# Performance work log

Measured on AMD Instinct MI355X. Metric: run time of the kernel, lower is better.

The kernel has to match this reference:

```python
import jax, jax.numpy as jnp
import numpy as np

H = 16  # num_heads
EPS = 1e-5

def _ln(x, g, b):
    m = jnp.mean(x, axis=-1, keepdims=True)
    v = jnp.var(x, axis=-1, keepdims=True)
    return (x - m) * jax.lax.rsqrt(v + EPS) * g + b

def setup_inputs() -> dict:
    key = jax.random.key(0)
    ks = jax.random.split(key, 4)
    B, N, C = 4, 1024, 1024
    D = C // H
    s_in = (2.0 / (C + 3 * C)) ** 0.5  # xavier-ish
    s_pr = (2.0 / (C + C)) ** 0.5
    return {
        "x": jax.random.normal(ks[0], (B, N, C), dtype=jnp.float32),
        "W_qkv": jax.random.normal(ks[1], (3 * C, C), dtype=jnp.float32) * s_in,
        "b_qkv": jnp.zeros((3 * C,), dtype=jnp.float32),
        "qn_g": jnp.ones((D,), dtype=jnp.float32),
        "qn_b": jnp.zeros((D,), dtype=jnp.float32),
        "kn_g": jnp.ones((D,), dtype=jnp.float32),
        "kn_b": jnp.zeros((D,), dtype=jnp.float32),
        "W_proj": jax.random.normal(ks[2], (C, C), dtype=jnp.float32) * s_pr,
        "b_proj": jnp.zeros((C,), dtype=jnp.float32),
    }

def reference(x, W_qkv, b_qkv, qn_g, qn_b, kn_g, kn_b, W_proj, b_proj):
    B, N, C = x.shape
    D = C // H
    scale = D ** -0.5
    qkv = x @ W_qkv.T + b_qkv                       # [B,N,3C]
    qkv = qkv.reshape(B, N, 3, H, D).transpose(2, 0, 3, 1, 4)  # [3,B,H,N,D]
    q, k, v = qkv[0], qkv[1], qkv[2]
    # source bug: qk_norm=(False,) is truthy -> LayerNorm applied to q and k
    q = _ln(q, qn_g, qn_b) * scale
    k = _ln(k, kn_g, kn_b)
    attn = jnp.einsum('bhnd,bhmd->bhnm', q, k)       # [B,H,N,N]
    weights = jax.nn.softmax(attn, axis=-1)
    out = jnp.einsum('bhnm,bhmd->bhnd', weights, v)  # [B,H,N,D]
    out = out.transpose(0, 2, 1, 3).reshape(B, N, C)
    out = out @ W_proj.T + b_proj
    return (out, weights)
```

## Files before the change

kernel.cpp:

```cpp
#include <hip/hip_runtime.h>
#include <math.h>

#define NH 16
#define HD 64
#define NB 4
#define SQ 1024
#define CH 1024

typedef _Float16 f16x8  __attribute__((ext_vector_type(8)));
typedef _Float16 f16x4  __attribute__((ext_vector_type(4)));
typedef float    f32x4  __attribute__((ext_vector_type(4)));

typedef const __attribute__((address_space(1))) void gvoid_t;
typedef __attribute__((address_space(3))) void lvoid_t;

#define NQ_X   (NB * SQ * CH / 4)
#define NQ_WQ  (3 * CH * CH / 4)
#define NQ_WP  (CH * CH / 4)
__global__ __launch_bounds__(256) void k_split_all(
    const float* __restrict__ x, const float* __restrict__ wqkv,
    const float* __restrict__ wp,
    _Float16* __restrict__ xf, _Float16* __restrict__ wqf,
    _Float16* __restrict__ wpf)
{
    int i = blockIdx.x * 256 + threadIdx.x;
    const float4 v = (i < NQ_X) ? ((const float4*)x)[i]
                   : (i < NQ_X + NQ_WQ) ? ((const float4*)wqkv)[i - NQ_X]
                   : ((const float4*)wp)[i - NQ_X - NQ_WQ];
    f16x4 h;
    h[0] = (_Float16)v.x; h[1] = (_Float16)v.y;
    h[2] = (_Float16)v.z; h[3] = (_Float16)v.w;
    if (i < NQ_X)             ((f16x4*)xf)[i] = h;
    else if (i < NQ_X + NQ_WQ)((f16x4*)wqf)[i - NQ_X] = h;
    else                      ((f16x4*)wpf)[i - NQ_X - NQ_WQ] = h;
}

template<int EPI>
__global__ __launch_bounds__(256) void k_mfma_gemm(
    const _Float16* __restrict__ A, const _Float16* __restrict__ B,
    const float* __restrict__ bias, float* __restrict__ outp,
    _Float16* __restrict__ qf, _Float16* __restrict__ kf, _Float16* __restrict__ vTf,
    const float* __restrict__ qg, const float* __restrict__ qb_,
    const float* __restrict__ kg, const float* __restrict__ kb_)
{
    __shared__ __align__(16) _Float16 sA[128 * 32];
    __shared__ __align__(16) _Float16 sB[128 * 32];

    const int tid = threadIdx.x;
    const int wid = tid >> 6, lane = tid & 63;
    const int wr = wid >> 1, wc = wid & 1;
    const int m0 = blockIdx.y * 128, n0 = blockIdx.x * 128;

    f32x4 acc[4][4];
    #pragma unroll
    for (int i = 0; i < 4; ++i)
        #pragma unroll
        for (int j = 0; j < 4; ++j)
            acc[i][j] = (f32x4){0.f, 0.f, 0.f, 0.f};

    const _Float16* gsrc = (wid < 2) ? A : B;
    _Float16* sdst = (wid < 2) ? sA : sB;
    const int gbase = (wid < 2) ? m0 : n0;
    const int ibase = (wid & 1) * 4;
    const int grow = gbase + (lane >> 2);
    const int gcol = (lane & 3) * 8;

    const int arow = wr * 64 + (lane & 15);
    const int brow = wc * 64 + (lane & 15);
    const int koff = (lane >> 4) * 8;

    for (int k0 = 0; k0 < CH; k0 += 32) {
        #pragma unroll
        for (int i = 0; i < 4; ++i) {
            const _Float16* g = gsrc + (size_t)(grow + (ibase + i) * 16) * CH + k0 + gcol;
            __builtin_amdgcn_global_load_lds((gvoid_t*)g,
                                             (lvoid_t*)(sdst + (ibase + i) * 512),
                                             16, 0, 0);
        }
        __syncthreads();

        f16x8 a[4], b[4];
        #pragma unroll
        for (int f = 0; f < 4; ++f) {
            a[f] = *(const f16x8*)&sA[(arow + f * 16) * 32 + koff];
            b[f] = *(const f16x8*)&sB[(brow + f * 16) * 32 + koff];
        }
        #pragma unroll
        for (int i = 0; i < 4; ++i)
            #pragma unroll
            for (int j = 0; j < 4; ++j)
                acc[i][j] = __builtin_amdgcn_mfma_f32_16x16x32_f16(a[i], b[j], acc[i][j], 0, 0, 0);
        __syncthreads();
    }

    const int crow = (lane >> 4) * 4;
    const int ccol = lane & 15;

    if (EPI == 1) {
        #pragma unroll
        for (int i = 0; i < 4; ++i) {
            #pragma unroll
            for (int j = 0; j < 4; ++j) {
                const int n = n0 + wc * 64 + j * 16 + ccol;
                const float bv = bias[n];
                #pragma unroll
                for (int r = 0; r < 4; ++r) {
                    const int m = m0 + wr * 64 + i * 16 + crow + r;
                    outp[(size_t)m * CH + n] = acc[i][j][r] + bv;
                }
            }
        }
    } else {
        const int nblk = n0 + wc * 64;
        const int sec = nblk >> 10;
        const int h = (nblk & 1023) >> 6;
        float bv[4];
        #pragma unroll
        for (int j = 0; j < 4; ++j) bv[j] = bias[nblk + j * 16 + ccol];

        if (sec < 2) {
            const float* gp = (sec == 0) ? qg : kg;
            const float* bp = (sec == 0) ? qb_ : kb_;
            float g4[4], b4[4];
            #pragma unroll
            for (int j = 0; j < 4; ++j) { g4[j] = gp[j*16+ccol]; b4[j] = bp[j*16+ccol]; }
            const float scale = (sec == 0) ? 0.125f : 1.0f;
            _Float16* dst = (sec == 0) ? qf : kf;
            #pragma unroll
            for (int i = 0; i < 4; ++i) {
                #pragma unroll
                for (int r = 0; r < 4; ++r) {
                    const int m = m0 + wr * 64 + i * 16 + crow + r;
                    const int b_ = m >> 10, nn = m & 1023;
                    float vals[4], s = 0.f, q2 = 0.f;
                    #pragma unroll
                    for (int j = 0; j < 4; ++j) {
                        vals[j] = acc[i][j][r] + bv[j];
                        s += vals[j]; q2 += vals[j] * vals[j];
                    }
                    #pragma unroll
                    for (int o = 1; o < 16; o <<= 1) {
                        s  += __shfl_xor(s, o, 64);
                        q2 += __shfl_xor(q2, o, 64);
                    }
                    const float mean = s * 0.015625f;
                    const float var = q2 * 0.015625f - mean * mean;
                    const float rstd = rsqrtf(var + 1e-5f);
                    #pragma unroll
                    for (int j = 0; j < 4; ++j) {
                        const float y = ((vals[j] - mean) * rstd * g4[j] + b4[j]) * scale;
                        dst[((size_t)(b_ * NH + h) * SQ + nn) * HD + j * 16 + ccol] = (_Float16)y;
                    }
                }
            }
        } else {
            #pragma unroll
            for (int i = 0; i < 4; ++i) {
                const int m0r = m0 + wr * 64 + i * 16 + crow;
                const int b_ = m0r >> 10, nn0 = m0r & 1023;
                #pragma unroll
                for (int j = 0; j < 4; ++j) {
                    f16x4 tmp;
                    #pragma unroll
                    for (int r = 0; r < 4; ++r) tmp[r] = (_Float16)(acc[i][j][r] + bv[j]);
                    *(f16x4*)&vTf[((size_t)(b_ * NH + h) * HD + j * 16 + ccol) * SQ + nn0] = tmp;
                }
            }
        }
    }
}

__global__ __launch_bounds__(256) void k_attn(
    const _Float16* __restrict__ q, const _Float16* __restrict__ k,
    const _Float16* __restrict__ vT, float* __restrict__ W,
    _Float16* __restrict__ opf)
{
    __shared__ _Float16 Pl[4][32][40];
    __shared__ float Of[4][32][72];
    const int L = blockIdx.x;
    const int bh   = (L & 7) * 8 + (L >> 6);
    const int xblk = (L >> 3) & 7;
    const int wid = threadIdx.x >> 6, lane = threadIdx.x & 63;
    const int row0 = xblk * 128 + wid * 32;
    const int lr = lane & 15, lg = lane >> 4;

    const _Float16* qh = q  + (size_t)bh * SQ * HD;
    const _Float16* kh = k  + (size_t)bh * SQ * HD;
    const _Float16* vh = vT + (size_t)bh * HD * SQ;

    f16x8 qb[2][2];
    #pragma unroll
    for (int qf = 0; qf < 2; ++qf)
        #pragma unroll
        for (int c = 0; c < 2; ++c)
            qb[qf][c] = *(const f16x8*)&qh[(size_t)(row0 + qf * 16 + lr) * HD + c * 32 + lg * 8];

    float lp0 = 0.f, lp1 = 0.f;
    #pragma unroll 4
    for (int kt = 0; kt < 64; ++kt) {
        const f16x8 ka0 = *(const f16x8*)&kh[(size_t)(kt * 16 + lr) * HD + lg * 8];
        const f16x8 ka1 = *(const f16x8*)&kh[(size_t)(kt * 16 + lr) * HD + 32 + lg * 8];
        f32x4 s0 = (f32x4){0.f, 0.f, 0.f, 0.f};
        f32x4 s1 = (f32x4){0.f, 0.f, 0.f, 0.f};
        s0 = __builtin_amdgcn_mfma_f32_16x16x32_f16(ka0, qb[0][0], s0, 0, 0, 0);
        s0 = __builtin_amdgcn_mfma_f32_16x16x32_f16(ka1, qb[0][1], s0, 0, 0, 0);
        s1 = __builtin_amdgcn_mfma_f32_16x16x32_f16(ka0, qb[1][0], s1, 0, 0, 0);
        s1 = __builtin_amdgcn_mfma_f32_16x16x32_f16(ka1, qb[1][1], s1, 0, 0, 0);
        #pragma unroll
        for (int r = 0; r < 4; ++r) { lp0 += __expf(s0[r]); lp1 += __expf(s1[r]); }
    }
    lp0 += __shfl_xor(lp0, 16, 64); lp0 += __shfl_xor(lp0, 32, 64);
    lp1 += __shfl_xor(lp1, 16, 64); lp1 += __shfl_xor(lp1, 32, 64);
    const float invl0 = 1.0f / lp0;
    const float invl1 = 1.0f / lp1;

    float* Wr = W + (size_t)bh * SQ * SQ;
    f32x4 opv[4][2];
    #pragma unroll
    for (int dt = 0; dt < 4; ++dt)
        #pragma unroll
        for (int qf = 0; qf < 2; ++qf)
            opv[dt][qf] = (f32x4){0.f, 0.f, 0.f, 0.f};

    for (int jc = 0; jc < 32; ++jc) {
        f16x8 vb[4];
        #pragma unroll
        for (int dt = 0; dt < 4; ++dt)
            vb[dt] = *(const f16x8*)&vh[(size_t)(dt * 16 + lr) * SQ + jc * 32 + lg * 8];

        #pragma unroll
        for (int t = 0; t < 2; ++t) {
            const int kt = jc * 2 + t;
            const f16x8 ka0 = *(const f16x8*)&kh[(size_t)(kt * 16 + lr) * HD + lg * 8];
            const f16x8 ka1 = *(const f16x8*)&kh[(size_t)(kt * 16 + lr) * HD + 32 + lg * 8];
            f32x4 s0 = (f32x4){0.f, 0.f, 0.f, 0.f};
            f32x4 s1 = (f32x4){0.f, 0.f, 0.f, 0.f};
            s0 = __builtin_amdgcn_mfma_f32_16x16x32_f16(ka0, qb[0][0], s0, 0, 0, 0);
            s0 = __builtin_amdgcn_mfma_f32_16x16x32_f16(ka1, qb[0][1], s0, 0, 0, 0);
            s1 = __builtin_amdgcn_mfma_f32_16x16x32_f16(ka0, qb[1][0], s1, 0, 0, 0);
            s1 = __builtin_amdgcn_mfma_f32_16x16x32_f16(ka1, qb[1][1], s1, 0, 0, 0);
            f32x4 wv0, wv1;
            f16x4 pv0, pv1;
            #pragma unroll
            for (int r = 0; r < 4; ++r) {
                wv0[r] = __expf(s0[r]) * invl0;  pv0[r] = (_Float16)wv0[r];
                wv1[r] = __expf(s1[r]) * invl1;  pv1[r] = (_Float16)wv1[r];
            }
            *(f32x4*)&Wr[(size_t)(row0 + lr) * SQ + kt * 16 + lg * 4]      = wv0;
            *(f32x4*)&Wr[(size_t)(row0 + 16 + lr) * SQ + kt * 16 + lg * 4] = wv1;
            *(f16x4*)&Pl[wid][lr][t * 16 + lg * 4]      = pv0;
            *(f16x4*)&Pl[wid][16 + lr][t * 16 + lg * 4] = pv1;
        }
        const f16x8 pa0 = *(const f16x8*)&Pl[wid][lr][lg * 8];
        const f16x8 pa1 = *(const f16x8*)&Pl[wid][16 + lr][lg * 8];
        #pragma unroll
        for (int dt = 0; dt < 4; ++dt) {
            opv[dt][0] = __builtin_amdgcn_mfma_f32_16x16x32_f16(pa0, vb[dt], opv[dt][0], 0, 0, 0);
            opv[dt][1] = __builtin_amdgcn_mfma_f32_16x16x32_f16(pa1, vb[dt], opv[dt][1], 0, 0, 0);
        }
    }

    #pragma unroll
    for (int dt = 0; dt < 4; ++dt)
        #pragma unroll
        for (int qf = 0; qf < 2; ++qf)
            #pragma unroll
            for (int r = 0; r < 4; ++r)
                Of[wid][qf * 16 + lg * 4 + r][dt * 16 + lr] = opv[dt][qf][r];
    const int b_ = bh >> 4, h = bh & 15;
    #pragma unroll
    for (int p = 0; p < 4; ++p) {
        const int r = p * 8 + (lane >> 3);
        const int c = (lane & 7) * 8;
        f16x8 hv;
        #pragma unroll
        for (int j = 0; j < 8; ++j)
            hv[j] = (_Float16)Of[wid][r][c + j];
        *(f16x8*)&opf[((size_t)(b_ * SQ + row0 + r)) * CH + h * HD + c] = hv;
    }
}

extern "C" void kernel_launch(void* const* d_in, const int* in_sizes, int n_in,
                              void* d_out, int out_size, void* d_ws, size_t ws_size,
                              hipStream_t stream)
{
    const float* x    = (const float*)d_in[0];
    const float* Wqkv = (const float*)d_in[1];
    const float* bqkv = (const float*)d_in[2];
    const float* qg   = (const float*)d_in[3];
    const float* qb   = (const float*)d_in[4];
    const float* kg   = (const float*)d_in[5];
    const float* kb   = (const float*)d_in[6];
    const float* Wp   = (const float*)d_in[7];
    const float* bp   = (const float*)d_in[8];

    float* out     = (float*)d_out;
    float* weights = out + (size_t)NB * SQ * CH;

    char* w = (char*)d_ws;
    _Float16* xf  = (_Float16*)w;
    _Float16* wqf = (_Float16*)(w + (((size_t)8)  << 20));
    _Float16* wpf = (_Float16*)(w + (((size_t)14) << 20));
    _Float16* qf  = (_Float16*)(w + (((size_t)16) << 20));
    _Float16* kf  = (_Float16*)(w + (((size_t)24) << 20));
    _Float16* vTf = (_Float16*)(w + (((size_t)32) << 20));
    _Float16* opf = (_Float16*)(w + (((size_t)40) << 20));

    k_split_all<<<dim3((NQ_X + NQ_WQ + NQ_WP) / 256), 256, 0, stream>>>(
        x, Wqkv, Wp, xf, wqf, wpf);

    k_mfma_gemm<0><<<dim3(24, 32), 256, 0, stream>>>(
        xf, wqf, bqkv, nullptr, qf, kf, vTf, qg, qb, kg, kb);

    k_attn<<<dim3(512), 256, 0, stream>>>(qf, kf, vTf, weights, opf);

    k_mfma_gemm<1><<<dim3(8, 32), 256, 0, stream>>>(
        opf, wpf, bp, out, nullptr, nullptr, nullptr,
        nullptr, nullptr, nullptr, nullptr);
}
```

Measured before the change: 195.9 us.

## Stage K and V chunks in LDS via direct global-to-LDS loads with XOR swizzle

Result: no change. 197.0 us (+0.5%).

```diff
diff --git a/kernel.cpp b/kernel.cpp
--- a/kernel.cpp
+++ b/kernel.cpp
@@ -175,14 +175,16 @@
     const _Float16* __restrict__ vT, float* __restrict__ W,
     _Float16* __restrict__ opf)
 {
-    __shared__ _Float16 Pl[4][32][40];
-    __shared__ float Of[4][32][72];
+    __shared__ __align__(16) char smem[75776];
+    _Float16* Kc = (_Float16*)smem;
+    _Float16* Vc = (_Float16*)(smem + 32768);
     const int L = blockIdx.x;
     const int bh   = (L & 7) * 8 + (L >> 6);
     const int xblk = (L >> 3) & 7;
     const int wid = threadIdx.x >> 6, lane = threadIdx.x & 63;
     const int row0 = xblk * 128 + wid * 32;
     const int lr = lane & 15, lg = lane >> 4;
+    _Float16* PlW = (_Float16*)(smem + 65536) + wid * 32 * 40;
 
     const _Float16* qh = q  + (size_t)bh * SQ * HD;
     const _Float16* kh = k  + (size_t)bh * SQ * HD;
@@ -222,51 +224,78 @@
         for (int qf = 0; qf < 2; ++qf)
             opv[dt][qf] = (f32x4){0.f, 0.f, 0.f, 0.f};
 
-    for (int jc = 0; jc < 32; ++jc) {
-        f16x8 vb[4];
-        #pragma unroll
-        for (int dt = 0; dt < 4; ++dt)
-            vb[dt] = *(const f16x8*)&vh[(size_t)(dt * 16 + lr) * SQ + jc * 32 + lg * 8];
-
-        #pragma unroll
-        for (int t = 0; t < 2; ++t) {
-            const int kt = jc * 2 + t;
-            const f16x8 ka0 = *(const f16x8*)&kh[(size_t)(kt * 16 + lr) * HD + lg * 8];
-            const f16x8 ka1 = *(const f16x8*)&kh[(size_t)(kt * 16 + lr) * HD + 32 + lg * 8];
-            f32x4 s0 = (f32x4){0.f, 0.f, 0.f, 0.f};
-            f32x4 s1 = (f32x4){0.f, 0.f, 0.f, 0.f};
-            s0 = __builtin_amdgcn_mfma_f32_16x16x32_f16(ka0, qb[0][0], s0, 0, 0, 0);
-            s0 = __builtin_amdgcn_mfma_f32_16x16x32_f16(ka1, qb[0][1], s0, 0, 0, 0);
-            s1 = __builtin_amdgcn_mfma_f32_16x16x32_f16(ka0, qb[1][0], s1, 0, 0, 0);
-            s1 = __builtin_amdgcn_mfma_f32_16x16x32_f16(ka1, qb[1][1], s1, 0, 0, 0);
-            f32x4 wv0, wv1;
-            f16x4 pv0, pv1;
-            #pragma unroll
-            for (int r = 0; r < 4; ++r) {
-                wv0[r] = __expf(s0[r]) * invl0;  pv0[r] = (_Float16)wv0[r];
-                wv1[r] = __expf(s1[r]) * invl1;  pv1[r] = (_Float16)wv1[r];
-            }
-            *(f32x4*)&Wr[(size_t)(row0 + lr) * SQ + kt * 16 + lg * 4]      = wv0;
-            *(f32x4*)&Wr[(size_t)(row0 + 16 + lr) * SQ + kt * 16 + lg * 4] = wv1;
-            *(f16x4*)&Pl[wid][lr][t * 16 + lg * 4]      = pv0;
-            *(f16x4*)&Pl[wid][16 + lr][t * 16 + lg * 4] = pv1;
-        }
-        const f16x8 pa0 = *(const f16x8*)&Pl[wid][lr][lg * 8];
-        const f16x8 pa1 = *(const f16x8*)&Pl[wid][16 + lr][lg * 8];
-        #pragma unroll
-        for (int dt = 0; dt < 4; ++dt) {
-            opv[dt][0] = __builtin_amdgcn_mfma_f32_16x16x32_f16(pa0, vb[dt], opv[dt][0], 0, 0, 0);
-            opv[dt][1] = __builtin_amdgcn_mfma_f32_16x16x32_f16(pa1, vb[dt], opv[dt][1], 0, 0, 0);
-        }
-    }
-
+    for (int kc = 0; kc < 4; ++kc) {
+        const _Float16* khc = kh + (size_t)kc * 256 * HD;
+        #pragma unroll
+        for (int i = 0; i < 8; ++i) {
+            const int krow = (wid * 8 + i) * 8 + (lane >> 3);
+            const int slot = lane & 7;
+            const _Float16* src = khc + (size_t)krow * HD + ((slot ^ (krow & 7)) * 8);
+            __builtin_amdgcn_global_load_lds((gvoid_t*)src,
+                (lvoid_t*)(Kc + (wid * 8 + i) * 512 + lane * 8), 16, 0, 0);
+        }
+        #pragma unroll
+        for (int i = 0; i < 8; ++i) {
+            const int vrow = (wid * 8 + i) * 2 + (lane >> 5);
+            const int slot = lane & 31;
+            const _Float16* src = vh + (size_t)vrow * SQ + kc * 256 + ((slot ^ (vrow & 7)) * 8);
+            __builtin_amdgcn_global_load_lds((gvoid_t*)src,
+                (lvoid_t*)(Vc + (wid * 8 + i) * 512 + lane * 8), 16, 0, 0);
+        }
+        __syncthreads();
+
+        for (int jcl = 0; jcl < 8; ++jcl) {
+            f16x8 vb[4];
+            #pragma unroll
+            for (int dt = 0; dt < 4; ++dt) {
+                const int vrow = dt * 16 + lr;
+                const int slot = (jcl * 4 + lg) ^ (vrow & 7);
+                vb[dt] = *(const f16x8*)&Vc[vrow * 256 + slot * 8];
+            }
+            #pragma unroll
+            for (int t = 0; t < 2; ++t) {
+                const int ktl = jcl * 2 + t;
+                const int kt = kc * 16 + ktl;
+                const int krow = ktl * 16 + lr;
+                const f16x8 ka0 = *(const f16x8*)&Kc[krow * 64 + ((lg ^ (krow & 7)) * 8)];
+                const f16x8 ka1 = *(const f16x8*)&Kc[krow * 64 + (((4 + lg) ^ (krow & 7)) * 8)];
+                f32x4 s0 = (f32x4){0.f, 0.f, 0.f, 0.f};
+                f32x4 s1 = (f32x4){0.f, 0.f, 0.f, 0.f};
+                s0 = __builtin_amdgcn_mfma_f32_16x16x32_f16(ka0, qb[0][0], s0, 0, 0, 0);
+                s0 = __builtin_amdgcn_mfma_f32_16x16x32_f16(ka1, qb[0][1], s0, 0, 0, 0);
+                s1 = __builtin_amdgcn_mfma_f32_16x16x32_f16(ka0, qb[1][0], s1, 0, 0, 0);
+                s1 = __builtin_amdgcn_mfma_f32_16x16x32_f16(ka1, qb[1][1], s1, 0, 0, 0);
+                f32x4 wv0, wv1;
+                f16x4 pv0, pv1;
+                #pragma unroll
+                for (int r = 0; r < 4; ++r) {
+                    wv0[r] = __expf(s0[r]) * invl0;  pv0[r] = (_Float16)wv0[r];
+                    wv1[r] = __expf(s1[r]) * invl1;  pv1[r] = (_Float16)wv1[r];
+                }
+                *(f32x4*)&Wr[(size_t)(row0 + lr) * SQ + kt * 16 + lg * 4]      = wv0;
+                *(f32x4*)&Wr[(size_t)(row0 + 16 + lr) * SQ + kt * 16 + lg * 4] = wv1;
+                *(f16x4*)&PlW[lr * 40 + t * 16 + lg * 4]        = pv0;
+                *(f16x4*)&PlW[(16 + lr) * 40 + t * 16 + lg * 4] = pv1;
+            }
+            const f16x8 pa0 = *(const f16x8*)&PlW[lr * 40 + lg * 8];
+            const f16x8 pa1 = *(const f16x8*)&PlW[(16 + lr) * 40 + lg * 8];
+            #pragma unroll
+            for (int dt = 0; dt < 4; ++dt) {
+                opv[dt][0] = __builtin_amdgcn_mfma_f32_16x16x32_f16(pa0, vb[dt], opv[dt][0], 0, 0, 0);
+                opv[dt][1] = __builtin_amdgcn_mfma_f32_16x16x32_f16(pa1, vb[dt], opv[dt][1], 0, 0, 0);
+            }
+        }
+        __syncthreads();
+    }
+
+    float* OfW = (float*)smem + wid * 32 * 72;
     #pragma unroll
     for (int dt = 0; dt < 4; ++dt)
         #pragma unroll
         for (int qf = 0; qf < 2; ++qf)
             #pragma unroll
             for (int r = 0; r < 4; ++r)
-                Of[wid][qf * 16 + lg * 4 + r][dt * 16 + lr] = opv[dt][qf][r];
+                OfW[(qf * 16 + lg * 4 + r) * 72 + dt * 16 + lr] = opv[dt][qf][r];
     const int b_ = bh >> 4, h = bh & 15;
     #pragma unroll
     for (int p = 0; p < 4; ++p) {
@@ -275,7 +304,7 @@
         f16x8 hv;
         #pragma unroll
         for (int j = 0; j < 8; ++j)
-            hv[j] = (_Float16)Of[wid][r][c + j];
+            hv[j] = (_Float16)OfW[r * 72 + c + j];
         *(f16x8*)&opf[((size_t)(b_ * SQ + row0 + r)) * CH + h * HD + c] = hv;
     }
 }
```
